# Performance work log

Measured on AMD Instinct MI355X. Metric: run time of the kernel, lower is better.

Reference implementation:

```python
import jax, jax.numpy as jnp
import numpy as np

D = 64        # dense voxel grid extent per axis
C = 256       # planes
R = 128       # planes // reduction
N = 100000    # number of occupied (unique) sparse voxels
K = 7         # max-pool kernel size
PAD = 3       # (K-1)//2, stride-1 'same' window


def setup_inputs() -> dict:
    key = jax.random.key(0)
    k1, k2, k3, k4 = jax.random.split(key, 4)
    feats = jax.random.normal(k1, (N, C), dtype=jnp.float32)
    # unique sparse coordinates in [0, D)^3 (MinkowskiEngine coords are unique)
    lin = jax.random.permutation(k2, D * D * D)[:N]
    coords = jnp.stack(jnp.unravel_index(lin, (D, D, D)), axis=-1).astype(jnp.int32)
    # 1x1 sparse convs == per-point linear layers (ME default bias=False)
    W1 = jax.random.normal(k3, (C, R), dtype=jnp.float32) * (1.0 / np.sqrt(C))
    W2 = jax.random.normal(k4, (R, C), dtype=jnp.float32) * (1.0 / np.sqrt(R))
    return {"feats": feats, "coords": coords, "W1": W1, "W2": W2}


def reference(feats, coords, W1, W2):
    neg_inf = jnp.array(-jnp.inf, dtype=feats.dtype)
    ix, iy, iz = coords[:, 0], coords[:, 1], coords[:, 2]
    # scatter sparse features into a dense grid; empty voxels = -inf so they
    grid = jnp.full((D, D, D, C), neg_inf, dtype=feats.dtype).at[ix, iy, iz].set(feats)
    # MinkowskiMaxPooling(kernel_size=7, stride=1): max over [-3,3]^3 window
    pooled = jax.lax.reduce_window(
        grid, neg_inf, jax.lax.max,
        window_dimensions=(K, K, K, 1),
        window_strides=(1, 1, 1, 1),
        padding=[(PAD, PAD), (PAD, PAD), (PAD, PAD), (0, 0)],
    )
    y = pooled[ix, iy, iz]  # [N, C], gather back to sparse points
    # fc: 1x1 conv -> ReLU -> 1x1 conv -> sigmoid (per-point MLP)
    y = jax.nn.sigmoid(jax.nn.relu(y @ W1) @ W2)
    return feats * y
```

## Files before the change

### kernel.cpp

```cpp
#include <hip/hip_runtime.h>
#include <hip/hip_bf16.h>

#define GD 64
#define GC 256

typedef unsigned short u16;
typedef unsigned int u32;
typedef short bf16x8 __attribute__((ext_vector_type(8)));
typedef float f32x4 __attribute__((ext_vector_type(4)));

__device__ __forceinline__ u16 f2bf_rne(float f) {
    u32 u = __builtin_bit_cast(u32, f);
    u = (u + 0x7FFFu + ((u >> 16) & 1u)) >> 16;
    return (u16)u;
}

__global__ __launch_bounds__(256) void init_grid(uint4* __restrict__ g, int n16) {
    int i = blockIdx.x * 256 + threadIdx.x;
    if (i < n16) {
        uint4 v;
        v.x = v.y = v.z = v.w = 0xFF80FF80u;
        g[i] = v;
    }
}

__global__ __launch_bounds__(256) void scatter_feats(const float* __restrict__ feats,
        const int* __restrict__ coords, u16* __restrict__ grid, int n) {
    int t = blockIdx.x * 256 + threadIdx.x;
    int i = t >> 5;
    if (i >= n) return;
    int c8 = (t & 31) << 3;
    int ix = coords[3 * i], iy = coords[3 * i + 1], iz = coords[3 * i + 2];
    size_t cell = (size_t)((ix * GD + iy) * GD + iz);
    const float4* src = (const float4*)(feats + (size_t)i * GC + c8);
    float4 a = src[0], b = src[1];
    u32 p0 = (u32)f2bf_rne(a.x) | ((u32)f2bf_rne(a.y) << 16);
    u32 p1 = (u32)f2bf_rne(a.z) | ((u32)f2bf_rne(a.w) << 16);
    u32 p2 = (u32)f2bf_rne(b.x) | ((u32)f2bf_rne(b.y) << 16);
    u32 p3 = (u32)f2bf_rne(b.z) | ((u32)f2bf_rne(b.w) << 16);
    uint4 v = make_uint4(p0, p1, p2, p3);
    *(uint4*)(grid + cell * GC + c8) = v;
}

__global__ __launch_bounds__(256) void prep_weights(const float* __restrict__ W1,
        const float* __restrict__ W2, u16* __restrict__ img1, u16* __restrict__ img2) {
    int t = blockIdx.x * 256 + threadIdx.x;
    if (t < 32768) {
        int h = t >> 14, nn = (t >> 8) & 63, chunk = (t >> 3) & 31, j = t & 7;
        int k = chunk * 8 + j;
        img1[(h << 14) + nn * 256 + (((chunk ^ (nn & 7)) << 3) | j)] =
            f2bf_rne(W1[k * 128 + h * 64 + nn]);
    } else {
        int t2 = t - 32768;
        int h = t2 >> 14, nn = (t2 >> 7) & 127, chunk = (t2 >> 3) & 15, j = t2 & 7;
        int k = chunk * 8 + j;
        img2[(h << 14) + nn * 128 + (((chunk ^ (nn & 7)) << 3) | j)] =
            f2bf_rne(W2[k * 256 + h * 128 + nn]);
    }
}

__device__ __forceinline__ void unpack8(uint4 r, float* w) {
    u32 v[4] = {r.x, r.y, r.z, r.w};
#pragma unroll
    for (int i = 0; i < 4; i++) {
        w[2 * i]     = __builtin_bit_cast(float, v[i] << 16);
        w[2 * i + 1] = __builtin_bit_cast(float, v[i] & 0xFFFF0000u);
    }
}

__global__ __launch_bounds__(256) void pool_pass_v(u16* __restrict__ grid,
        int mulA, int mulB, int strideCell) {
    int chunk = threadIdx.x & 31;
    int L = blockIdx.x * 8 + (threadIdx.x >> 5);
    int a = L >> 6, b = L & 63;
    size_t baseEl = ((size_t)a * mulA + (size_t)b * mulB) * GC + chunk * 8;
    size_t stepEl = (size_t)strideCell * GC;
    u16* p = grid + baseEl;

    float win[7][8];
#pragma unroll
    for (int s = 0; s < 7; s++)
#pragma unroll
        for (int c = 0; c < 8; c++) win[s][c] = -INFINITY;

#pragma unroll
    for (int t = 0; t < 3; t++) {
        uint4 r = *(const uint4*)(p + (size_t)t * stepEl);
        unpack8(r, win[t + 3]);
    }

#pragma unroll
    for (int z = 0; z < 64; z++) {
        int slot = (z + 6) % 7;
        if (z + 3 < 64) {
            uint4 r = *(const uint4*)(p + (size_t)(z + 3) * stepEl);
            unpack8(r, win[slot]);
        } else {
#pragma unroll
            for (int c = 0; c < 8; c++) win[slot][c] = -INFINITY;
        }
        u32 q[4];
#pragma unroll
        for (int i = 0; i < 4; i++) {
            u32 halves[2];
#pragma unroll
            for (int hh = 0; hh < 2; hh++) {
                int c = 2 * i + hh;
                float m01 = fmaxf(win[0][c], win[1][c]);
                float m23 = fmaxf(win[2][c], win[3][c]);
                float m45 = fmaxf(win[4][c], win[5][c]);
                float m = fmaxf(fmaxf(m01, m23), fmaxf(m45, win[6][c]));
                halves[hh] = __builtin_bit_cast(u32, m);
            }
            q[i] = (halves[0] >> 16) | (halves[1] & 0xFFFF0000u);
        }
        *(uint4*)(p + (size_t)z * stepEl) = make_uint4(q[0], q[1], q[2], q[3]);
    }
}

__global__ __launch_bounds__(256, 4) void gemm1_kernel(const u16* __restrict__ grid,
        const int* __restrict__ coords, const u16* __restrict__ img1,
        u16* __restrict__ H, int n, int nrb) {
    __shared__ __align__(16) u16 w1t[64 * 256];
    int h = blockIdx.x >= nrb;
    int rb = blockIdx.x - (h ? nrb : 0);
    int tid = threadIdx.x;

    const uint4* src = (const uint4*)(img1 + (h << 14));
    uint4* dst = (uint4*)w1t;
#pragma unroll
    for (int i = 0; i < 8; i++) dst[i * 256 + tid] = src[i * 256 + tid];

    int wave = tid >> 6, lane = tid & 63, m16 = lane & 15, quad = lane >> 4;
    int row_a = rb * 64 + wave * 16 + m16;
    int ra = min(row_a, n - 1);
    int ix = coords[3 * ra], iy = coords[3 * ra + 1], iz = coords[3 * ra + 2];
    const u16* yrow = grid + (size_t)((ix * GD + iy) * GD + iz) * GC;
    bf16x8 afr[8];
#pragma unroll
    for (int kk = 0; kk < 8; kk++)
        afr[kk] = *(const bf16x8*)(yrow + kk * 32 + quad * 8);
    __syncthreads();

    f32x4 acc[4];
#pragma unroll
    for (int t = 0; t < 4; t++) acc[t] = (f32x4){0.f, 0.f, 0.f, 0.f};
#pragma unroll
    for (int kk = 0; kk < 8; kk++) {
        int chunk = kk * 4 + quad;
#pragma unroll
        for (int t = 0; t < 4; t++) {
            int r = t * 16 + m16;
            bf16x8 b = *(const bf16x8*)&w1t[r * 256 + ((chunk ^ (r & 7)) << 3)];
            acc[t] = __builtin_amdgcn_mfma_f32_16x16x32_bf16(afr[kk], b, acc[t], 0, 0, 0);
        }
    }
    __syncthreads();

    u16* hbuf = w1t;
#pragma unroll
    for (int t = 0; t < 4; t++) {
        int col = t * 16 + m16;
        int c8 = col >> 3, j = col & 7;
#pragma unroll
        for (int rr = 0; rr < 4; rr++) {
            int row_l = wave * 16 + quad * 4 + rr;
            float hv = fmaxf(acc[t][rr], 0.0f);
            hbuf[row_l * 64 + (((c8 ^ (row_l & 7)) << 3) | j)] = f2bf_rne(hv);
        }
    }
    __syncthreads();
#pragma unroll
    for (int i = 0; i < 2; i++) {
        int cid = i * 256 + tid;
        int row_l = cid >> 3, c8 = cid & 7;
        int grow = rb * 64 + row_l;
        if (grow < n) {
            bf16x8 v = *(const bf16x8*)&hbuf[row_l * 64 + ((c8 ^ (row_l & 7)) << 3)];
            *(bf16x8*)&H[(size_t)grow * 128 + h * 64 + c8 * 8] = v;
        }
    }
}

__global__ __launch_bounds__(256, 4) void gemm2_kernel(const u16* __restrict__ H,
        const u16* __restrict__ img2, const float* __restrict__ feats,
        float* __restrict__ out, int n, int nrb) {
    __shared__ __align__(16) char smem[64 * 140 * 4];
    u16* w2t = (u16*)smem;
    float* zbuf = (float*)smem;
    int h = blockIdx.x >= nrb;
    int rb = blockIdx.x - (h ? nrb : 0);
    int tid = threadIdx.x;

    const uint4* src = (const uint4*)(img2 + (h << 14));
    uint4* dst = (uint4*)w2t;
#pragma unroll
    for (int i = 0; i < 8; i++) dst[i * 256 + tid] = src[i * 256 + tid];

    int wave = tid >> 6, lane = tid & 63, m16 = lane & 15, quad = lane >> 4;
    int row_a = rb * 64 + wave * 16 + m16;
    int ra = min(row_a, n - 1);
    const u16* hrow = H + (size_t)ra * 128;
    bf16x8 afr[4];
#pragma unroll
    for (int kk = 0; kk < 4; kk++)
        afr[kk] = *(const bf16x8*)(hrow + kk * 32 + quad * 8);
    __syncthreads();

    f32x4 acc[8];
#pragma unroll
    for (int t = 0; t < 8; t++) acc[t] = (f32x4){0.f, 0.f, 0.f, 0.f};
#pragma unroll
    for (int kk = 0; kk < 4; kk++) {
        int chunk = kk * 4 + quad;
#pragma unroll
        for (int t = 0; t < 8; t++) {
            int nn = t * 16 + m16;
            bf16x8 b = *(const bf16x8*)&w2t[nn * 128 + ((chunk ^ (nn & 7)) << 3)];
            acc[t] = __builtin_amdgcn_mfma_f32_16x16x32_bf16(afr[kk], b, acc[t], 0, 0, 0);
        }
    }
    __syncthreads();

#pragma unroll
    for (int t = 0; t < 8; t++) {
        int col = t * 16 + m16;
#pragma unroll
        for (int rr = 0; rr < 4; rr++) {
            int row_l = wave * 16 + quad * 4 + rr;
            zbuf[row_l * 140 + col] = acc[t][rr];
        }
    }
    __syncthreads();
#pragma unroll
    for (int i = 0; i < 8; i++) {
        int f = i * 256 + tid;
        int row_l = f >> 5, c4 = f & 31;
        int grow = rb * 64 + row_l;
        if (grow < n) {
            f32x4 z = *(const f32x4*)&zbuf[row_l * 140 + c4 * 4];
            size_t o = (size_t)grow * 256 + h * 128 + c4 * 4;
            f32x4 ft = *(const f32x4*)&feats[o];
            f32x4 r;
#pragma unroll
            for (int c = 0; c < 4; c++)
                r[c] = ft[c] / (1.0f + __expf(-z[c]));
            *(f32x4*)&out[o] = r;
        }
    }
}

extern "C" void kernel_launch(void* const* d_in, const int* in_sizes, int n_in,
                              void* d_out, int out_size, void* d_ws, size_t ws_size,
                              hipStream_t stream) {
    const float* feats = (const float*)d_in[0];
    const int* coords = (const int*)d_in[1];
    const float* W1 = (const float*)d_in[2];
    const float* W2 = (const float*)d_in[3];
    float* out = (float*)d_out;

    int n = in_sizes[1] / 3;

    size_t grid_bytes = (size_t)GD * GD * GD * GC * 2;
    u16* grid = (u16*)d_ws;
    u16* H = (u16*)((char*)d_ws + grid_bytes);
    u16* img1 = (u16*)((char*)d_ws + grid_bytes + (size_t)n * 128 * 2);
    u16* img2 = img1 + 32768;

    int n16 = (int)(grid_bytes / 16);
    init_grid<<<n16 / 256, 256, 0, stream>>>((uint4*)d_ws, n16);

    prep_weights<<<256, 256, 0, stream>>>(W1, W2, img1, img2);

    scatter_feats<<<(n * 32 + 255) / 256, 256, 0, stream>>>(feats, coords, grid, n);

    pool_pass_v<<<512, 256, 0, stream>>>(grid, GD * GD, GD, 1);
    pool_pass_v<<<512, 256, 0, stream>>>(grid, GD * GD, 1, GD);
    pool_pass_v<<<512, 256, 0, stream>>>(grid, GD, 1, GD * GD);

    int nrb = (n + 63) / 64;
    gemm1_kernel<<<2 * nrb, 256, 0, stream>>>(grid, coords, img1, H, n, nrb);
    gemm2_kernel<<<2 * nrb, 256, 0, stream>>>(H, img2, feats, out, n, nrb);
}
```

Baseline: 380.5 us.

## Replace grid init with occupancy bitmask and ping-pong pooling buffers

Removes the full-grid -inf initialization kernel and instead records an occupancy bitmask per (x,y) column during scatter. The first pooling pass reads only occupied cells from the stale buffer and treats the rest as -inf, writing into a second buffer; the later passes ping-pong between the two grids. This saves a 32 MB memset and skips loads of empty voxels in the first pass, at the cost of doubling workspace, adding atomics on the mask, and giving up in-place updates.

```diff
diff --git a/kernel.cpp b/kernel.cpp
--- a/kernel.cpp
+++ b/kernel.cpp
@@ -6,6 +6,7 @@
 
 typedef unsigned short u16;
 typedef unsigned int u32;
+typedef unsigned long long u64;
 typedef short bf16x8 __attribute__((ext_vector_type(8)));
 typedef float f32x4 __attribute__((ext_vector_type(4)));
 
@@ -15,36 +16,11 @@
     return (u16)u;
 }
 
-__global__ __launch_bounds__(256) void init_grid(uint4* __restrict__ g, int n16) {
-    int i = blockIdx.x * 256 + threadIdx.x;
-    if (i < n16) {
-        uint4 v;
-        v.x = v.y = v.z = v.w = 0xFF80FF80u;
-        g[i] = v;
-    }
-}
-
-__global__ __launch_bounds__(256) void scatter_feats(const float* __restrict__ feats,
-        const int* __restrict__ coords, u16* __restrict__ grid, int n) {
+__global__ __launch_bounds__(256) void prep_weights(const float* __restrict__ W1,
+        const float* __restrict__ W2, u16* __restrict__ img1, u16* __restrict__ img2,
+        u64* __restrict__ maskZ) {
     int t = blockIdx.x * 256 + threadIdx.x;
-    int i = t >> 5;
-    if (i >= n) return;
-    int c8 = (t & 31) << 3;
-    int ix = coords[3 * i], iy = coords[3 * i + 1], iz = coords[3 * i + 2];
-    size_t cell = (size_t)((ix * GD + iy) * GD + iz);
-    const float4* src = (const float4*)(feats + (size_t)i * GC + c8);
-    float4 a = src[0], b = src[1];
-    u32 p0 = (u32)f2bf_rne(a.x) | ((u32)f2bf_rne(a.y) << 16);
-    u32 p1 = (u32)f2bf_rne(a.z) | ((u32)f2bf_rne(a.w) << 16);
-    u32 p2 = (u32)f2bf_rne(b.x) | ((u32)f2bf_rne(b.y) << 16);
-    u32 p3 = (u32)f2bf_rne(b.z) | ((u32)f2bf_rne(b.w) << 16);
-    uint4 v = make_uint4(p0, p1, p2, p3);
-    *(uint4*)(grid + cell * GC + c8) = v;
-}
-
-__global__ __launch_bounds__(256) void prep_weights(const float* __restrict__ W1,
-        const float* __restrict__ W2, u16* __restrict__ img1, u16* __restrict__ img2) {
-    int t = blockIdx.x * 256 + threadIdx.x;
+    if (t < 4096) maskZ[t] = 0ull;
     if (t < 32768) {
         int h = t >> 14, nn = (t >> 8) & 63, chunk = (t >> 3) & 31, j = t & 7;
         int k = chunk * 8 + j;
@@ -59,6 +35,25 @@
     }
 }
 
+__global__ __launch_bounds__(256) void scatter_feats(const float* __restrict__ feats,
+        const int* __restrict__ coords, u16* __restrict__ gridA,
+        u64* __restrict__ maskZ, int n) {
+    int t = blockIdx.x * 256 + threadIdx.x;
+    int i = t >> 5;
+    if (i >= n) return;
+    int c8 = (t & 31) << 3;
+    int ix = coords[3 * i], iy = coords[3 * i + 1], iz = coords[3 * i + 2];
+    if ((t & 31) == 0) atomicOr(&maskZ[ix * GD + iy], 1ull << iz);
+    size_t cell = (size_t)((ix * GD + iy) * GD + iz);
+    const float4* src = (const float4*)(feats + (size_t)i * GC + c8);
+    float4 a = src[0], b = src[1];
+    u32 p0 = (u32)f2bf_rne(a.x) | ((u32)f2bf_rne(a.y) << 16);
+    u32 p1 = (u32)f2bf_rne(a.z) | ((u32)f2bf_rne(a.w) << 16);
+    u32 p2 = (u32)f2bf_rne(b.x) | ((u32)f2bf_rne(b.y) << 16);
+    u32 p3 = (u32)f2bf_rne(b.z) | ((u32)f2bf_rne(b.w) << 16);
+    *(uint4*)(gridA + cell * GC + c8) = make_uint4(p0, p1, p2, p3);
+}
+
 __device__ __forceinline__ void unpack8(uint4 r, float* w) {
     u32 v[4] = {r.x, r.y, r.z, r.w};
 #pragma unroll
@@ -68,14 +63,18 @@
     }
 }
 
-__global__ __launch_bounds__(256) void pool_pass_v(u16* __restrict__ grid,
+template<bool MASKED>
+__global__ __launch_bounds__(256, 2) void pool_pass_pp(const u16* __restrict__ src,
+        u16* __restrict__ dst, const u64* __restrict__ maskZ,
         int mulA, int mulB, int strideCell) {
     int chunk = threadIdx.x & 31;
     int L = blockIdx.x * 8 + (threadIdx.x >> 5);
     int a = L >> 6, b = L & 63;
     size_t baseEl = ((size_t)a * mulA + (size_t)b * mulB) * GC + chunk * 8;
     size_t stepEl = (size_t)strideCell * GC;
-    u16* p = grid + baseEl;
+    const u16* ps = src + baseEl;
+    u16* pd = dst + baseEl;
+    u64 m = MASKED ? maskZ[L] : 0ull;
 
     float win[7][8];
 #pragma unroll
@@ -85,15 +84,18 @@
 
 #pragma unroll
     for (int t = 0; t < 3; t++) {
-        uint4 r = *(const uint4*)(p + (size_t)t * stepEl);
-        unpack8(r, win[t + 3]);
+        if (!MASKED || ((m >> t) & 1)) {
+            uint4 r = *(const uint4*)(ps + (size_t)t * stepEl);
+            unpack8(r, win[t + 3]);
+        }
     }
 
 #pragma unroll
     for (int z = 0; z < 64; z++) {
         int slot = (z + 6) % 7;
-        if (z + 3 < 64) {
-            uint4 r = *(const uint4*)(p + (size_t)(z + 3) * stepEl);
+        bool ld = (z + 3 < 64) && (!MASKED || ((m >> (z + 3)) & 1));
+        if (ld) {
+            uint4 r = *(const uint4*)(ps + (size_t)(z + 3) * stepEl);
             unpack8(r, win[slot]);
         } else {
 #pragma unroll
@@ -109,12 +111,12 @@
                 float m01 = fmaxf(win[0][c], win[1][c]);
                 float m23 = fmaxf(win[2][c], win[3][c]);
                 float m45 = fmaxf(win[4][c], win[5][c]);
-                float m = fmaxf(fmaxf(m01, m23), fmaxf(m45, win[6][c]));
-                halves[hh] = __builtin_bit_cast(u32, m);
+                float mx = fmaxf(fmaxf(m01, m23), fmaxf(m45, win[6][c]));
+                halves[hh] = __builtin_bit_cast(u32, mx);
             }
             q[i] = (halves[0] >> 16) | (halves[1] & 0xFFFF0000u);
         }
-        *(uint4*)(p + (size_t)z * stepEl) = make_uint4(q[0], q[1], q[2], q[3]);
+        *(uint4*)(pd + (size_t)z * stepEl) = make_uint4(q[0], q[1], q[2], q[3]);
     }
 }
 
@@ -262,23 +264,23 @@
     int n = in_sizes[1] / 3;
 
     size_t grid_bytes = (size_t)GD * GD * GD * GC * 2;
-    u16* grid = (u16*)d_ws;
-    u16* H = (u16*)((char*)d_ws + grid_bytes);
-    u16* img1 = (u16*)((char*)d_ws + grid_bytes + (size_t)n * 128 * 2);
-    u16* img2 = img1 + 32768;
-
-    int n16 = (int)(grid_bytes / 16);
-    init_grid<<<n16 / 256, 256, 0, stream>>>((uint4*)d_ws, n16);
-
-    prep_weights<<<256, 256, 0, stream>>>(W1, W2, img1, img2);
-
-    scatter_feats<<<(n * 32 + 255) / 256, 256, 0, stream>>>(feats, coords, grid, n);
-
-    pool_pass_v<<<512, 256, 0, stream>>>(grid, GD * GD, GD, 1);
-    pool_pass_v<<<512, 256, 0, stream>>>(grid, GD * GD, 1, GD);
-    pool_pass_v<<<512, 256, 0, stream>>>(grid, GD, 1, GD * GD);
+    u16* A = (u16*)d_ws;
+    u16* B = (u16*)((char*)d_ws + grid_bytes);
+    char* p = (char*)d_ws + 2 * grid_bytes;
+    u16* H = (u16*)p;                   p += (size_t)n * 128 * 2;
+    u16* img1 = (u16*)p;                p += 65536 * 2;
+    u16* img2 = (u16*)p;                p += 65536 * 2;
+    u64* maskZ = (u64*)p;
+
+    prep_weights<<<256, 256, 0, stream>>>(W1, W2, img1, img2, maskZ);
+
+    scatter_feats<<<(n * 32 + 255) / 256, 256, 0, stream>>>(feats, coords, A, maskZ, n);
+
+    pool_pass_pp<true ><<<512, 256, 0, stream>>>(A, B, maskZ, GD * GD, GD, 1);
+    pool_pass_pp<false><<<512, 256, 0, stream>>>(B, A, maskZ, GD * GD, 1, GD);
+    pool_pass_pp<false><<<512, 256, 0, stream>>>(A, B, maskZ, GD, 1, GD * GD);
 
     int nrb = (n + 63) / 64;
-    gemm1_kernel<<<2 * nrb, 256, 0, stream>>>(grid, coords, img1, H, n, nrb);
+    gemm1_kernel<<<2 * nrb, 256, 0, stream>>>(B, coords, img1, H, n, nrb);
     gemm2_kernel<<<2 * nrb, 256, 0, stream>>>(H, img2, feats, out, n, nrb);
 }
```

Result: no change. 386.5 us (+1.6%).
